# Optimization experiments

Hardware: AMD Instinct MI355X
Metric: run time of the kernel (lower is better)

Reference implementation:

```python
import jax, jax.numpy as jnp
import numpy as np

B, S, D, H = 2, 2048, 1024, 16
HEAD_DIM = D // H
SCALE = HEAD_DIM ** -0.5


def setup_inputs() -> dict:
    key = jax.random.key(0)
    k1, k2, k3 = jax.random.split(key, 3)
    x = jax.random.normal(k1, (B, S, D), dtype=jnp.float32)
    # torch nn.Linear convention: weight is [out_features, in_features], y = x @ W.T + b
    W_qkv = jax.random.normal(k2, (3 * D, D), dtype=jnp.float32) * 0.02  # qkv Linear, bias=False
    W_out = jax.random.normal(k3, (D, D), dtype=jnp.float32) * 0.02
    b_out = jnp.zeros((D,), dtype=jnp.float32)
    return {"x": x, "W_qkv": W_qkv, "W_out": W_out, "b_out": b_out}


def reference(x, W_qkv, W_out, b_out):
    b, s, d_model = x.shape
    # qkv projection (no bias), then split 'b c (qkv h d) -> qkv b h c d'
    qkv = (x @ W_qkv.T).reshape(b, s, 3, H, HEAD_DIM).transpose(2, 0, 3, 1, 4)
    q, k, v = qkv[0], qkv[1], qkv[2]  # each [b, h, s, hd]
    # naive full attention: scores materialized as [b, h, s, s]
    attn = jax.nn.softmax(jnp.einsum('bhxd,bhyd->bhxy', q, k) * SCALE, axis=-1)
    # dropout is identity (rate 0 / eval mode)
    o = jnp.einsum('bhxy,bhyd->bhxd', attn, v)
    o = o.transpose(0, 2, 1, 3).reshape(b, s, d_model)  # 'b h c d -> b c (h d)'
    return o @ W_out.T + b_out
```

## Files before the change

### kernel.cpp

```cpp
#include <hip/hip_runtime.h>


typedef __attribute__((ext_vector_type(8))) short short8;
typedef __attribute__((ext_vector_type(4))) float f32x4;
typedef __attribute__((ext_vector_type(2))) unsigned int uint32x2;
typedef unsigned short ushort_t;
typedef unsigned int uint32;

#define AS1 __attribute__((address_space(1)))
#define AS3 __attribute__((address_space(3)))

__device__ __forceinline__ void gload_lds16(const void* gp, void* lp) {
    __builtin_amdgcn_global_load_lds((const AS1 void*)gp, (AS3 void*)lp, 16, 0, 0);
}

#if __has_builtin(__builtin_amdgcn_exp2f)
#define EXP2F(x) __builtin_amdgcn_exp2f(x)
#else
#define EXP2F(x) exp2f(x)
#endif

__device__ __forceinline__ uint32 rhu(float f) { return __float_as_uint(f) + 0x8000u; }
#if __has_builtin(__builtin_amdgcn_perm)
__device__ __forceinline__ uint32 pk2bf(float a, float b) {
    return __builtin_amdgcn_perm(rhu(b), rhu(a), 0x07060302u);
}
#else
__device__ __forceinline__ uint32 pk2bf(float a, float b) {
    return (rhu(a) >> 16) | (rhu(b) & 0xffff0000u);
}
#endif
__device__ __forceinline__ ushort_t f2bf(float f) { return (ushort_t)(rhu(f) >> 16); }

#if __has_builtin(__builtin_amdgcn_permlane32_swap)
__device__ __forceinline__ void plane32(uint32& a, uint32& b) {
    uint32x2 r = __builtin_amdgcn_permlane32_swap(a, b, false, false);
    a = r[0]; b = r[1];
}
#else
__device__ __forceinline__ void plane32(uint32& a, uint32& b) {
    asm("v_permlane32_swap_b32 %0, %1" : "+v"(a), "+v"(b));
}
#endif
#if __has_builtin(__builtin_amdgcn_permlane16_swap)
__device__ __forceinline__ void plane16(uint32& a, uint32& b) {
    uint32x2 r = __builtin_amdgcn_permlane16_swap(a, b, false, false);
    a = r[0]; b = r[1];
}
#else
__device__ __forceinline__ void plane16(uint32& a, uint32& b) {
    asm("v_permlane16_swap_b32 %0, %1" : "+v"(a), "+v"(b));
}
#endif

__global__ void cvt_all(const float* __restrict__ x, ushort_t* __restrict__ xb,
                        const float* __restrict__ wq, ushort_t* __restrict__ wqb,
                        const float* __restrict__ wo, ushort_t* __restrict__ wob) {
    int blk = blockIdx.x;
    const float* in; ushort_t* out;
    if (blk < 4096)      { in = x;  out = xb;  }
    else if (blk < 7168) { in = wq; out = wqb; blk -= 4096; }
    else                 { in = wo; out = wob; blk -= 7168; }
    const int i = (blk * 256 + threadIdx.x) * 4;
    const float4 v = *(const float4*)(in + i);
    uint2 pk;
    pk.x = pk2bf(v.x, v.y);
    pk.y = pk2bf(v.z, v.w);
    *(uint2*)(out + i) = pk;
}

__global__ __launch_bounds__(256, 2)
void gemm_qkv(const ushort_t* __restrict__ A, const ushort_t* __restrict__ B,
              ushort_t* __restrict__ Cb, ushort_t* __restrict__ vT,
              int M, int N, int K, int ldc, float qScale) {
    __shared__ ushort_t lA[2][128 * 32];
    __shared__ ushort_t lB[2][128 * 32];
    const int tid = threadIdx.x;
    const int wave = tid >> 6, lane = tid & 63;
    const int quad = lane >> 4, l16 = lane & 15;
    const int wr = wave >> 1, wc = wave & 1;
    const int mBase = blockIdx.y * 128, nBase = blockIdx.x * 128;

    f32x4 acc[4][4];
#pragma unroll
    for (int i = 0; i < 4; i++)
#pragma unroll
        for (int j = 0; j < 4; j++) acc[i][j] = (f32x4){0.f, 0.f, 0.f, 0.f};

    const int ar = tid >> 2;
    const int ac = (((tid & 3) ^ ((ar >> 1) & 3)) * 8);
    const int rsw = ((l16 >> 1) & 3);

    const ushort_t* aptr = A + (size_t)(mBase + ar) * K + ac;
    const ushort_t* bptr = B + (size_t)(nBase + ar) * K + ac;

#define G1_STAGE(buf, k0)                                                            \
    {                                                                                \
        _Pragma("unroll") for (int c = 0; c < 2; c++) {                              \
            gload_lds16(aptr + (size_t)(c * 64) * K + (k0), lA[buf] + c * 2048 + wave * 512); \
            gload_lds16(bptr + (size_t)(c * 64) * K + (k0), lB[buf] + c * 2048 + wave * 512); \
        }                                                                            \
    }

    G1_STAGE(0, 0);
    for (int k0 = 0; k0 < K; k0 += 32) {
        const int cur = (k0 >> 5) & 1;
        __syncthreads();
        if (k0 + 32 < K) G1_STAGE(cur ^ 1, k0 + 32);

        short8 af[4], bf[4];
#pragma unroll
        for (int i = 0; i < 4; i++)
            af[i] = *(const short8*)(lA[cur] + (wr * 64 + i * 16 + l16) * 32 + ((quad ^ rsw) * 8));
#pragma unroll
        for (int j = 0; j < 4; j++)
            bf[j] = *(const short8*)(lB[cur] + (wc * 64 + j * 16 + l16) * 32 + ((quad ^ rsw) * 8));
#pragma unroll
        for (int i = 0; i < 4; i++)
#pragma unroll
            for (int j = 0; j < 4; j++)
                acc[i][j] = __builtin_amdgcn_mfma_f32_16x16x32_bf16(af[i], bf[j], acc[i][j], 0, 0, 0);
    }

    if (nBase >= 2048) {
#pragma unroll
        for (int i = 0; i < 4; i++)
#pragma unroll
            for (int j = 0; j < 4; j++) {
                const int row0 = mBase + wr * 64 + i * 16 + quad * 4;
                const int col = nBase + wc * 64 + j * 16 + l16 - 2048;
                const int b = row0 >> 11, s0 = row0 & 2047;
                uint2 pk;
                pk.x = pk2bf(acc[i][j][0], acc[i][j][1]);
                pk.y = pk2bf(acc[i][j][2], acc[i][j][3]);
                *(uint2*)(vT + ((size_t)(b * 16) * 64 + col) * 2048 + s0) = pk;
            }
        return;
    }
    const float cs = (nBase < 1024) ? qScale : 1.0f;
#pragma unroll
    for (int i = 0; i < 4; i++)
#pragma unroll
        for (int j = 0; j < 4; j++)
#pragma unroll
            for (int r = 0; r < 4; r++) {
                const int row = mBase + wr * 64 + i * 16 + quad * 4 + r;
                const int col = nBase + wc * 64 + j * 16 + l16;
                Cb[(size_t)row * ldc + col] = f2bf(acc[i][j][r] * cs);
            }
}

__global__ __launch_bounds__(256, 2)
void gemm_out(const ushort_t* __restrict__ A, const ushort_t* __restrict__ B,
              float* __restrict__ Cf, const float* __restrict__ bias,
              int M, int N, int K) {
    __shared__ ushort_t lA[2][64 * 64];
    __shared__ ushort_t lB[2][128 * 64];
    const int tid = threadIdx.x;
    const int wave = tid >> 6, lane = tid & 63;
    const int quad = lane >> 4, l16 = lane & 15;
    const int mBase = blockIdx.y * 64, nBase = blockIdx.x * 128;

    f32x4 acc[4][2];
#pragma unroll
    for (int i = 0; i < 4; i++)
#pragma unroll
        for (int j = 0; j < 2; j++) acc[i][j] = (f32x4){0.f, 0.f, 0.f, 0.f};

    const int sr = tid >> 3;
    const int sc = ((tid & 7) ^ (sr & 7)) * 8;
    const int swz = l16 & 7;

    const ushort_t* aptr = A + (size_t)(mBase + sr) * K + sc;
    const ushort_t* bptr = B + (size_t)(nBase + sr) * K + sc;

#define G2_STAGE(buf, k0)                                                              \
    {                                                                                  \
        _Pragma("unroll") for (int c = 0; c < 2; c++)                                  \
            gload_lds16(aptr + (size_t)(c * 32) * K + (k0), lA[buf] + c * 2048 + wave * 512); \
        _Pragma("unroll") for (int c = 0; c < 4; c++)                                  \
            gload_lds16(bptr + (size_t)(c * 32) * K + (k0), lB[buf] + c * 2048 + wave * 512); \
    }

    G2_STAGE(0, 0);
    for (int k0 = 0; k0 < K; k0 += 64) {
        const int cur = (k0 >> 6) & 1;
        __syncthreads();
        if (k0 + 64 < K) G2_STAGE(cur ^ 1, k0 + 64);

#pragma unroll
        for (int ks = 0; ks < 2; ks++) {
            short8 af[4], bf[2];
#pragma unroll
            for (int i = 0; i < 4; i++)
                af[i] = *(const short8*)(lA[cur] + (i * 16 + l16) * 64 + (((ks * 4 + quad) ^ swz) * 8));
#pragma unroll
            for (int j = 0; j < 2; j++)
                bf[j] = *(const short8*)(lB[cur] + (wave * 32 + j * 16 + l16) * 64 + (((ks * 4 + quad) ^ swz) * 8));
#pragma unroll
            for (int i = 0; i < 4; i++)
#pragma unroll
                for (int j = 0; j < 2; j++)
                    acc[i][j] = __builtin_amdgcn_mfma_f32_16x16x32_bf16(af[i], bf[j], acc[i][j], 0, 0, 0);
        }
    }

#pragma unroll
    for (int i = 0; i < 4; i++)
#pragma unroll
        for (int j = 0; j < 2; j++)
#pragma unroll
            for (int r = 0; r < 4; r++) {
                const int row = mBase + i * 16 + quad * 4 + r;
                const int col = nBase + wave * 32 + j * 16 + l16;
                Cf[(size_t)row * N + col] = acc[i][j][r] + bias[col];
            }
}

__global__ __launch_bounds__(512, 4)
void attn_flash(const ushort_t* __restrict__ qk, const ushort_t* __restrict__ vT,
                ushort_t* __restrict__ o) {
    __shared__ ushort_t smem[28672];

    const int tid = threadIdx.x;
    const int wave = tid >> 6, lane = tid & 63;
    const int quad = lane >> 4, l16 = lane & 15;
    const int qg = wave & 3, kg = wave >> 2;
    const int bh = blockIdx.x, b = bh >> 4, h = bh & 15;
    const size_t rowBase = (size_t)b * 2048;
    const int qCol = h * 64, kCol = 1024 + h * 64;
    const int qRow0 = blockIdx.y * 128;
    const int swz = l16 & 7;

    const int sr = tid >> 3;
    const int sc = ((tid & 7) ^ (sr & 7)) * 8;

#pragma unroll
    for (int cc = 0; cc < 2; cc++)
        gload_lds16(qk + (rowBase + qRow0 + cc * 64 + sr) * 2048 + qCol + sc,
                    smem + 20480 + cc * 4096 + wave * 512);
    __syncthreads();
    short8 qf[2][2];
#pragma unroll
    for (int qt = 0; qt < 2; qt++)
#pragma unroll
        for (int ks = 0; ks < 2; ks++)
            qf[qt][ks] = *(const short8*)(smem + 20480 + (qg * 32 + qt * 16 + l16) * 64 +
                                          (((ks * 4 + quad) ^ swz) * 8));

    short8 onesA;
#pragma unroll
    for (int i = 0; i < 8; i++) onesA[i] = (short)0x3F80;

    f32x4 oacc[4][2];
    f32x4 lacc[2];
#pragma unroll
    for (int qt = 0; qt < 2; qt++) {
        lacc[qt] = (f32x4){0.f, 0.f, 0.f, 0.f};
#pragma unroll
        for (int dt = 0; dt < 4; dt++) oacc[dt][qt] = (f32x4){0.f, 0.f, 0.f, 0.f};
    }

    const ushort_t* kptr = qk + (rowBase + sr) * 2048 + kCol + sc;
    const ushort_t* vptr = vT + ((size_t)bh * 64 + sr) * 2048 + sc;

    f32x4 sacc[2][2];
    short8 pfA[2], pfB[2];

#define AT_STAGE(kbi, vbi, kt)                                                         \
    {                                                                                  \
        gload_lds16(kptr + (size_t)((kt) * 64) * 2048, smem + (kbi) * 4096 + wave * 512); \
        gload_lds16(vptr + (kt) * 64, smem + 8192 + (vbi) * 4096 + wave * 512);        \
    }

#define S_BLOCK(cur)                                                                   \
    {                                                                                  \
        const ushort_t* lK = smem + (cur) * 4096;                                      \
        _Pragma("unroll") for (int mh = 0; mh < 2; mh++) {                             \
            const int krow = kg * 32 + mh * 16 + l16;                                  \
            const short8 k0 = *(const short8*)(lK + krow * 64 + ((quad ^ swz) * 8));   \
            const short8 k1 = *(const short8*)(lK + krow * 64 + (((4 + quad) ^ swz) * 8)); \
            __builtin_amdgcn_s_setprio(1);                                             \
            _Pragma("unroll") for (int qt = 0; qt < 2; qt++) {                         \
                f32x4 t = (f32x4){0.f, 0.f, 0.f, 0.f};                                 \
                t = __builtin_amdgcn_mfma_f32_16x16x32_bf16(k0, qf[qt][0], t, 0, 0, 0); \
                t = __builtin_amdgcn_mfma_f32_16x16x32_bf16(k1, qf[qt][1], t, 0, 0, 0); \
                sacc[mh][qt] = t;                                                      \
            }                                                                          \
            __builtin_amdgcn_s_setprio(0);                                             \
        }                                                                              \
    }

#define EXPPK_BLOCK(pfdst)                                                             \
    _Pragma("unroll") for (int qt = 0; qt < 2; qt++) {                                 \
        uint32 a0 = pk2bf(EXP2F(sacc[0][qt][0]), EXP2F(sacc[0][qt][1]));               \
        uint32 a1 = pk2bf(EXP2F(sacc[0][qt][2]), EXP2F(sacc[0][qt][3]));               \
        uint32 b0 = pk2bf(EXP2F(sacc[1][qt][0]), EXP2F(sacc[1][qt][1]));               \
        uint32 b1 = pk2bf(EXP2F(sacc[1][qt][2]), EXP2F(sacc[1][qt][3]));               \
        plane32(a0, b0); plane16(a0, b0);                                              \
        plane32(a1, b1); plane16(a1, b1);                                              \
        union { uint32 u[4]; short8 s; } w_;                                           \
        w_.u[0] = a0; w_.u[1] = a1; w_.u[2] = b0; w_.u[3] = b1;                        \
        pfdst[qt] = w_.s;                                                              \
    }

#define PV_BLOCK(vbi, pf)                                                              \
    {                                                                                  \
        const ushort_t* lV = smem + 8192 + (vbi) * 4096;                               \
        _Pragma("unroll") for (int qt = 0; qt < 2; qt++)                               \
            lacc[qt] = __builtin_amdgcn_mfma_f32_16x16x32_bf16(onesA, pf[qt], lacc[qt], 0, 0, 0); \
        __builtin_amdgcn_s_setprio(1);                                                 \
        _Pragma("unroll") for (int dt = 0; dt < 4; dt++) {                             \
            const short8 vf = *(const short8*)(lV + (dt * 16 + l16) * 64 +             \
                                               (((kg * 4 + quad) ^ swz) * 8));         \
            _Pragma("unroll") for (int qt = 0; qt < 2; qt++)                           \
                oacc[dt][qt] = __builtin_amdgcn_mfma_f32_16x16x32_bf16(vf, pf[qt], oacc[dt][qt], 0, 0, 0); \
        }                                                                              \
        __builtin_amdgcn_s_setprio(0);                                                 \
    }

    AT_STAGE(0, 0, 0);

    __syncthreads();
    AT_STAGE(1, 1, 1);
    S_BLOCK(0);
    EXPPK_BLOCK(pfA);

    int vs = 2;
    int vp = 0;
    for (int kt = 1; kt <= 29; kt += 2) {
        __syncthreads();
        AT_STAGE(0, vs, kt + 1);
        S_BLOCK(1);
        PV_BLOCK(vp, pfA);
        EXPPK_BLOCK(pfB);
        vs = (vs == 2) ? 0 : vs + 1;
        vp = (vp == 2) ? 0 : vp + 1;
        __syncthreads();
        AT_STAGE(1, vs, kt + 2);
        S_BLOCK(0);
        PV_BLOCK(vp, pfB);
        EXPPK_BLOCK(pfA);
        vs = (vs == 2) ? 0 : vs + 1;
        vp = (vp == 2) ? 0 : vp + 1;
    }

    __syncthreads();
    S_BLOCK(1);
    PV_BLOCK(0, pfA);
    EXPPK_BLOCK(pfB);
    PV_BLOCK(1, pfB);

    __syncthreads();
    float* red = (float*)smem;
    if (kg == 1) {
#pragma unroll
        for (int qt = 0; qt < 2; qt++) {
            if (quad == 0) red[8192 + qg * 32 + qt * 16 + l16] = lacc[qt][0];
#pragma unroll
            for (int dt = 0; dt < 4; dt++)
                *(f32x4*)(red + (((qg * 4 + dt) * 2 + qt) * 64 + lane) * 4) = oacc[dt][qt];
        }
    }
    __syncthreads();
    if (kg == 0) {
        float linv[2];
#pragma unroll
        for (int qt = 0; qt < 2; qt++)
            linv[qt] = 1.0f / (lacc[qt][0] + red[8192 + qg * 32 + qt * 16 + l16]);
#pragma unroll
        for (int qt = 0; qt < 2; qt++) {
            const size_t row = rowBase + qRow0 + qg * 32 + qt * 16 + l16;
#pragma unroll
            for (int dt = 0; dt < 4; dt++) {
                const f32x4 r = *(const f32x4*)(red + (((qg * 4 + dt) * 2 + qt) * 64 + lane) * 4);
                uint2 pk;
                pk.x = pk2bf((oacc[dt][qt][0] + r[0]) * linv[qt],
                             (oacc[dt][qt][1] + r[1]) * linv[qt]);
                pk.y = pk2bf((oacc[dt][qt][2] + r[2]) * linv[qt],
                             (oacc[dt][qt][3] + r[3]) * linv[qt]);
                *(uint2*)(o + row * 1024 + h * 64 + dt * 16 + quad * 4) = pk;
            }
        }
    }
}

extern "C" void kernel_launch(void* const* d_in, const int* in_sizes, int n_in,
                              void* d_out, int out_size, void* d_ws, size_t ws_size,
                              hipStream_t stream) {
    const float* x    = (const float*)d_in[0];
    const float* Wqkv = (const float*)d_in[1];
    const float* Wout = (const float*)d_in[2];
    const float* bout = (const float*)d_in[3];
    float* out = (float*)d_out;

    ushort_t* xb    = (ushort_t*)d_ws;
    ushort_t* wqkvb = xb + (size_t)4096 * 1024;
    ushort_t* woutb = wqkvb + (size_t)3072 * 1024;
    ushort_t* qkb   = woutb + (size_t)1024 * 1024;
    ushort_t* vTb   = qkb + (size_t)4096 * 2048;
    ushort_t* ob    = xb;

    const float SC = 0.125f * 1.44269504089f;

    cvt_all<<<8192, 256, 0, stream>>>(x, xb, Wqkv, wqkvb, Wout, woutb);
    gemm_qkv<<<dim3(24, 32), 256, 0, stream>>>(xb, wqkvb, qkb, vTb, 4096, 3072, 1024, 2048, SC);
    attn_flash<<<dim3(32, 16), 512, 0, stream>>>(qkb, vTb, ob);
    gemm_out<<<dim3(8, 64), 256, 0, stream>>>(ob, woutb, out, bout, 4096, 1024, 1024);
}
```

Baseline: 172.8 us.

## Halve attention block to 4 waves/64 queries and simplify to double-buffered loop

The attention kernel now uses 256-thread blocks that each handle 64 query rows, with twice as many blocks and a smaller LDS footprint. This should allow more blocks per CU and better load balance. The previous software pipeline, which overlapped the next tile's PV with the current S and used triple-buffered V, is replaced by a simple double-buffered loop: S, then exp, then PV. That removes the cross-iteration overlap of softmax with MFMA work, and each K/V tile is now loaded by twice as many blocks.

```diff
diff --git a/kernel.cpp b/kernel.cpp
--- a/kernel.cpp
+++ b/kernel.cpp
@@ -217,36 +217,37 @@
             }
 }
 
-__global__ __launch_bounds__(512, 4)
+__global__ __launch_bounds__(256, 4)
 void attn_flash(const ushort_t* __restrict__ qk, const ushort_t* __restrict__ vT,
                 ushort_t* __restrict__ o) {
-    __shared__ ushort_t smem[28672];
+    __shared__ ushort_t smem[16384];
 
     const int tid = threadIdx.x;
     const int wave = tid >> 6, lane = tid & 63;
     const int quad = lane >> 4, l16 = lane & 15;
-    const int qg = wave & 3, kg = wave >> 2;
+    const int qg = wave & 1, kg = wave >> 1;
     const int bh = blockIdx.x, b = bh >> 4, h = bh & 15;
     const size_t rowBase = (size_t)b * 2048;
     const int qCol = h * 64, kCol = 1024 + h * 64;
-    const int qRow0 = blockIdx.y * 128;
+    const int qRow0 = blockIdx.y * 64;
     const int swz = l16 & 7;
 
-    const int sr = tid >> 3;
-    const int sc = ((tid & 7) ^ (sr & 7)) * 8;
+    const int sr0 = tid >> 3;
+    const int sc = ((tid & 7) ^ (sr0 & 7)) * 8;
 
 #pragma unroll
     for (int cc = 0; cc < 2; cc++)
-        gload_lds16(qk + (rowBase + qRow0 + cc * 64 + sr) * 2048 + qCol + sc,
-                    smem + 20480 + cc * 4096 + wave * 512);
+        gload_lds16(qk + (rowBase + qRow0 + cc * 32 + sr0) * 2048 + qCol + sc,
+                    smem + cc * 2048 + wave * 512);
     __syncthreads();
     short8 qf[2][2];
 #pragma unroll
     for (int qt = 0; qt < 2; qt++)
 #pragma unroll
         for (int ks = 0; ks < 2; ks++)
-            qf[qt][ks] = *(const short8*)(smem + 20480 + (qg * 32 + qt * 16 + l16) * 64 +
+            qf[qt][ks] = *(const short8*)(smem + (qg * 32 + qt * 16 + l16) * 64 +
                                           (((ks * 4 + quad) ^ swz) * 8));
+    __syncthreads();
 
     short8 onesA;
 #pragma unroll
@@ -261,16 +262,20 @@
         for (int dt = 0; dt < 4; dt++) oacc[dt][qt] = (f32x4){0.f, 0.f, 0.f, 0.f};
     }
 
-    const ushort_t* kptr = qk + (rowBase + sr) * 2048 + kCol + sc;
-    const ushort_t* vptr = vT + ((size_t)bh * 64 + sr) * 2048 + sc;
+    const ushort_t* kptr = qk + (rowBase + sr0) * 2048 + kCol + sc;
+    const ushort_t* vptr = vT + ((size_t)bh * 64 + sr0) * 2048 + sc;
 
     f32x4 sacc[2][2];
-    short8 pfA[2], pfB[2];
-
-#define AT_STAGE(kbi, vbi, kt)                                                         \
+    short8 pf[2];
+
+#define AT_STAGE(buf, kt)                                                              \
     {                                                                                  \
-        gload_lds16(kptr + (size_t)((kt) * 64) * 2048, smem + (kbi) * 4096 + wave * 512); \
-        gload_lds16(vptr + (kt) * 64, smem + 8192 + (vbi) * 4096 + wave * 512);        \
+        _Pragma("unroll") for (int cc = 0; cc < 2; cc++) {                             \
+            gload_lds16(kptr + (size_t)((kt) * 64 + cc * 32) * 2048,                   \
+                        smem + (buf) * 4096 + cc * 2048 + wave * 512);                 \
+            gload_lds16(vptr + (size_t)(cc * 32) * 2048 + (kt) * 64,                   \
+                        smem + 8192 + (buf) * 4096 + cc * 2048 + wave * 512);          \
+        }                                                                              \
     }
 
 #define S_BLOCK(cur)                                                                   \
@@ -304,59 +309,37 @@
         pfdst[qt] = w_.s;                                                              \
     }
 
-#define PV_BLOCK(vbi, pf)                                                              \
+#define PV_BLOCK(cur, pfv)                                                             \
     {                                                                                  \
-        const ushort_t* lV = smem + 8192 + (vbi) * 4096;                               \
+        const ushort_t* lV = smem + 8192 + (cur) * 4096;                               \
         _Pragma("unroll") for (int qt = 0; qt < 2; qt++)                               \
-            lacc[qt] = __builtin_amdgcn_mfma_f32_16x16x32_bf16(onesA, pf[qt], lacc[qt], 0, 0, 0); \
+            lacc[qt] = __builtin_amdgcn_mfma_f32_16x16x32_bf16(onesA, pfv[qt], lacc[qt], 0, 0, 0); \
         __builtin_amdgcn_s_setprio(1);                                                 \
         _Pragma("unroll") for (int dt = 0; dt < 4; dt++) {                             \
             const short8 vf = *(const short8*)(lV + (dt * 16 + l16) * 64 +             \
                                                (((kg * 4 + quad) ^ swz) * 8));         \
             _Pragma("unroll") for (int qt = 0; qt < 2; qt++)                           \
-                oacc[dt][qt] = __builtin_amdgcn_mfma_f32_16x16x32_bf16(vf, pf[qt], oacc[dt][qt], 0, 0, 0); \
+                oacc[dt][qt] = __builtin_amdgcn_mfma_f32_16x16x32_bf16(vf, pfv[qt], oacc[dt][qt], 0, 0, 0); \
         }                                                                              \
         __builtin_amdgcn_s_setprio(0);                                                 \
     }
 
-    AT_STAGE(0, 0, 0);
-
-    __syncthreads();
-    AT_STAGE(1, 1, 1);
-    S_BLOCK(0);
-    EXPPK_BLOCK(pfA);
-
-    int vs = 2;
-    int vp = 0;
-    for (int kt = 1; kt <= 29; kt += 2) {
+    AT_STAGE(0, 0);
+    for (int kt = 0; kt < 32; kt++) {
+        const int cur = kt & 1;
         __syncthreads();
-        AT_STAGE(0, vs, kt + 1);
-        S_BLOCK(1);
-        PV_BLOCK(vp, pfA);
-        EXPPK_BLOCK(pfB);
-        vs = (vs == 2) ? 0 : vs + 1;
-        vp = (vp == 2) ? 0 : vp + 1;
-        __syncthreads();
-        AT_STAGE(1, vs, kt + 2);
-        S_BLOCK(0);
-        PV_BLOCK(vp, pfB);
-        EXPPK_BLOCK(pfA);
-        vs = (vs == 2) ? 0 : vs + 1;
-        vp = (vp == 2) ? 0 : vp + 1;
-    }
-
-    __syncthreads();
-    S_BLOCK(1);
-    PV_BLOCK(0, pfA);
-    EXPPK_BLOCK(pfB);
-    PV_BLOCK(1, pfB);
+        if (kt < 31) AT_STAGE(cur ^ 1, kt + 1);
+        S_BLOCK(cur);
+        EXPPK_BLOCK(pf);
+        PV_BLOCK(cur, pf);
+    }
 
     __syncthreads();
     float* red = (float*)smem;
     if (kg == 1) {
 #pragma unroll
         for (int qt = 0; qt < 2; qt++) {
-            if (quad == 0) red[8192 + qg * 32 + qt * 16 + l16] = lacc[qt][0];
+            if (quad == 0) red[4096 + qg * 32 + qt * 16 + l16] = lacc[qt][0];
 #pragma unroll
             for (int dt = 0; dt < 4; dt++)
                 *(f32x4*)(red + (((qg * 4 + dt) * 2 + qt) * 64 + lane) * 4) = oacc[dt][qt];
@@ -367,7 +350,7 @@
         float linv[2];
 #pragma unroll
         for (int qt = 0; qt < 2; qt++)
-            linv[qt] = 1.0f / (lacc[qt][0] + red[8192 + qg * 32 + qt * 16 + l16]);
+            linv[qt] = 1.0f / (lacc[qt][0] + red[4096 + qg * 32 + qt * 16 + l16]);
 #pragma unroll
         for (int qt = 0; qt < 2; qt++) {
             const size_t row = rowBase + qRow0 + qg * 32 + qt * 16 + l16;
@@ -405,6 +388,6 @@
 
     cvt_all<<<8192, 256, 0, stream>>>(x, xb, Wqkv, wqkvb, Wout, woutb);
     gemm_qkv<<<dim3(24, 32), 256, 0, stream>>>(xb, wqkvb, qkb, vTb, 4096, 3072, 1024, 2048, SC);
-    attn_flash<<<dim3(32, 16), 512, 0, stream>>>(qkb, vTb, ob);
+    attn_flash<<<dim3(32, 32), 256, 0, stream>>>(qkb, vTb, ob);
     gemm_out<<<dim3(8, 64), 256, 0, stream>>>(ob, woutb, out, bout, 4096, 1024, 1024);
 }
```

After: 176.8 us. +2.3%, slower.

## Enlarge QKV GEMM tile to 256x256 with 4-stage LDS pipeline and block swizzle

Applied to the files above, without the earlier changes.

The QKV projection GEMM moves from 128x128 tiles with 4 waves and double buffering to 256x256 tiles with 8 waves, a 4-deep global-to-LDS prefetch ring using explicit vmcnt waits, and a remapped block index meant to improve L2 locality. Larger tiles raise operand reuse per LDS load, and the deeper pipeline hides global memory latency better. In exchange the grid drops to 192 blocks, which can underfill the GPU's compute units, and the doubled accumulator set raises register pressure. Sizes are now hardcoded.

```diff
diff --git a/kernel.cpp b/kernel.cpp
--- a/kernel.cpp
+++ b/kernel.cpp
@@ -69,65 +69,84 @@
     *(uint2*)(out + i) = pk;
 }
 
-__global__ __launch_bounds__(256, 2)
+__global__ __launch_bounds__(512, 2)
 void gemm_qkv(const ushort_t* __restrict__ A, const ushort_t* __restrict__ B,
-              ushort_t* __restrict__ Cb, ushort_t* __restrict__ vT,
-              int M, int N, int K, int ldc, float qScale) {
-    __shared__ ushort_t lA[2][128 * 32];
-    __shared__ ushort_t lB[2][128 * 32];
+              ushort_t* __restrict__ Cb, ushort_t* __restrict__ vT, float qScale) {
+    __shared__ ushort_t smem[4][16384];
+    const int K = 1024;
     const int tid = threadIdx.x;
     const int wave = tid >> 6, lane = tid & 63;
     const int quad = lane >> 4, l16 = lane & 15;
-    const int wr = wave >> 1, wc = wave & 1;
-    const int mBase = blockIdx.y * 128, nBase = blockIdx.x * 128;
-
-    f32x4 acc[4][4];
-#pragma unroll
-    for (int i = 0; i < 4; i++)
+    const int wr = wave >> 2, wc = wave & 3;
+
+    int bid = blockIdx.x + 12 * blockIdx.y;
+    bid = (bid & 7) * 24 + (bid >> 3);
+    const int nBase = (bid % 12) * 256, mBase = (bid / 12) * 256;
+
+    f32x4 acc[8][4];
+#pragma unroll
+    for (int i = 0; i < 8; i++)
 #pragma unroll
         for (int j = 0; j < 4; j++) acc[i][j] = (f32x4){0.f, 0.f, 0.f, 0.f};
 
     const int ar = tid >> 2;
-    const int ac = (((tid & 3) ^ ((ar >> 1) & 3)) * 8);
-    const int rsw = ((l16 >> 1) & 3);
+    const int ac = ((tid & 3) ^ ((ar >> 1) & 3)) * 8;
+    const int rsw = (l16 >> 1) & 3;
 
     const ushort_t* aptr = A + (size_t)(mBase + ar) * K + ac;
     const ushort_t* bptr = B + (size_t)(nBase + ar) * K + ac;
 
-#define G1_STAGE(buf, k0)                                                            \
-    {                                                                                \
-        _Pragma("unroll") for (int c = 0; c < 2; c++) {                              \
-            gload_lds16(aptr + (size_t)(c * 64) * K + (k0), lA[buf] + c * 2048 + wave * 512); \
-            gload_lds16(bptr + (size_t)(c * 64) * K + (k0), lB[buf] + c * 2048 + wave * 512); \
-        }                                                                            \
-    }
-
-    G1_STAGE(0, 0);
-    for (int k0 = 0; k0 < K; k0 += 32) {
-        const int cur = (k0 >> 5) & 1;
-        __syncthreads();
-        if (k0 + 32 < K) G1_STAGE(cur ^ 1, k0 + 32);
-
-        short8 af[4], bf[4];
-#pragma unroll
-        for (int i = 0; i < 4; i++)
-            af[i] = *(const short8*)(lA[cur] + (wr * 64 + i * 16 + l16) * 32 + ((quad ^ rsw) * 8));
-#pragma unroll
-        for (int j = 0; j < 4; j++)
-            bf[j] = *(const short8*)(lB[cur] + (wc * 64 + j * 16 + l16) * 32 + ((quad ^ rsw) * 8));
-#pragma unroll
-        for (int i = 0; i < 4; i++)
-#pragma unroll
-            for (int j = 0; j < 4; j++)
-                acc[i][j] = __builtin_amdgcn_mfma_f32_16x16x32_bf16(af[i], bf[j], acc[i][j], 0, 0, 0);
-    }
+#define G1_STAGE(t)                                                                   \
+    {                                                                                 \
+        ushort_t* d = &smem[(t) & 3][0];                                              \
+        const int k0 = (t) * 32;                                                      \
+        gload_lds16(aptr + k0, d + wave * 512);                                       \
+        gload_lds16(aptr + (size_t)128 * K + k0, d + 4096 + wave * 512);              \
+        gload_lds16(bptr + k0, d + 8192 + wave * 512);                                \
+        gload_lds16(bptr + (size_t)128 * K + k0, d + 12288 + wave * 512);             \
+    }
+
+#define G1_COMPUTE(t)                                                                 \
+    {                                                                                 \
+        const ushort_t* lA = &smem[(t) & 3][0];                                       \
+        const ushort_t* lB = lA + 8192;                                               \
+        short8 af[8], bf[4];                                                          \
+        _Pragma("unroll") for (int i = 0; i < 8; i++)                                 \
+            af[i] = *(const short8*)(lA + (wr * 128 + i * 16 + l16) * 32 +            \
+                                     ((quad ^ rsw) * 8));                             \
+        _Pragma("unroll") for (int j = 0; j < 4; j++)                                 \
+            bf[j] = *(const short8*)(lB + (wc * 64 + j * 16 + l16) * 32 +             \
+                                     ((quad ^ rsw) * 8));                             \
+        _Pragma("unroll") for (int i = 0; i < 8; i++)                                 \
+            _Pragma("unroll") for (int j = 0; j < 4; j++)                             \
+                acc[i][j] = __builtin_amdgcn_mfma_f32_16x16x32_bf16(af[i], bf[j],     \
+                                                                    acc[i][j], 0, 0, 0); \
+    }
+
+#define G1_SYNC(n)                                                                    \
+    asm volatile("s_waitcnt vmcnt(" #n ")" ::: "memory");                             \
+    __builtin_amdgcn_s_barrier();                                                     \
+    asm volatile("" ::: "memory");
+
+    G1_STAGE(0); G1_STAGE(1); G1_STAGE(2);
+
+#pragma unroll 4
+    for (int t = 0; t < 28; ++t) {
+        G1_SYNC(8);
+        G1_STAGE(t + 3);
+        G1_COMPUTE(t);
+    }
+    { G1_SYNC(8); G1_STAGE(31); G1_COMPUTE(28); }
+    { G1_SYNC(8); G1_COMPUTE(29); }
+    { G1_SYNC(4); G1_COMPUTE(30); }
+    { G1_SYNC(0); G1_COMPUTE(31); }
 
     if (nBase >= 2048) {
 #pragma unroll
-        for (int i = 0; i < 4; i++)
+        for (int i = 0; i < 8; i++)
 #pragma unroll
             for (int j = 0; j < 4; j++) {
-                const int row0 = mBase + wr * 64 + i * 16 + quad * 4;
+                const int row0 = mBase + wr * 128 + i * 16 + quad * 4;
                 const int col = nBase + wc * 64 + j * 16 + l16 - 2048;
                 const int b = row0 >> 11, s0 = row0 & 2047;
                 uint2 pk;
@@ -139,14 +158,14 @@
     }
     const float cs = (nBase < 1024) ? qScale : 1.0f;
 #pragma unroll
-    for (int i = 0; i < 4; i++)
+    for (int i = 0; i < 8; i++)
 #pragma unroll
         for (int j = 0; j < 4; j++)
 #pragma unroll
             for (int r = 0; r < 4; r++) {
-                const int row = mBase + wr * 64 + i * 16 + quad * 4 + r;
+                const int row = mBase + wr * 128 + i * 16 + quad * 4 + r;
                 const int col = nBase + wc * 64 + j * 16 + l16;
-                Cb[(size_t)row * ldc + col] = f2bf(acc[i][j][r] * cs);
+                Cb[(size_t)row * 2048 + col] = f2bf(acc[i][j][r] * cs);
             }
 }
 
@@ -326,8 +345,7 @@
     S_BLOCK(0);
     EXPPK_BLOCK(pfA);
 
-    int vs = 2;
-    int vp = 0;
+    int vs = 2, vp = 0;
     for (int kt = 1; kt <= 29; kt += 2) {
         __syncthreads();
         AT_STAGE(0, vs, kt + 1);
@@ -404,7 +422,7 @@
     const float SC = 0.125f * 1.44269504089f;
 
     cvt_all<<<8192, 256, 0, stream>>>(x, xb, Wqkv, wqkvb, Wout, woutb);
-    gemm_qkv<<<dim3(24, 32), 256, 0, stream>>>(xb, wqkvb, qkb, vTb, 4096, 3072, 1024, 2048, SC);
+    gemm_qkv<<<dim3(12, 16), 512, 0, stream>>>(xb, wqkvb, qkb, vTb, SC);
     attn_flash<<<dim3(32, 16), 512, 0, stream>>>(qkb, vTb, ob);
     gemm_out<<<dim3(8, 64), 256, 0, stream>>>(ob, woutb, out, bout, 4096, 1024, 1024);
 }
```

Measured after the change: 170.1 us (median of 2 runs). No clear change (-1.5%).
